# Performance work log

Hardware: AMD Instinct MI355X
Metric: run time of the kernel (lower is better)

Reference implementation:

```python
import jax, jax.numpy as jnp
import numpy as np

B, C, IC, H, W = 16, 256, 128, 32, 32  # batch, in_channels, inter_channels, spatial
EPS = 1e-5


def _conv1x1(x, w, b=None):
    # x: [B,C,H,W], w: [O,C] -> [B,O,H,W]
    y = jnp.einsum('bchw,oc->bohw', x, w)
    if b is not None:
        y = y + b[None, :, None, None]
    return y


def _dot_kernel(x, wt, wp):
    # relu-matmul attention, symmetrized, degree-rsqrt normalized with zero masking
    b, _, h, w = x.shape
    n = h * w
    t = jnp.maximum(_conv1x1(x, wt), 0.0).reshape(b, -1, n)  # [B,IC,N]
    p = jnp.maximum(_conv1x1(x, wp), 0.0).reshape(b, -1, n)  # [B,IC,N]
    att = jnp.einsum('bcn,bcm->bnm', t, p)                    # [B,N,N]
    att = (att + att.transpose(0, 2, 1)) * 0.5
    d = att.sum(axis=2)                                       # [B,N]
    dinv = jnp.where(d != 0, jax.lax.rsqrt(jnp.where(d != 0, d, 1.0)), 0.0)
    return att * dinv[:, None, :] * dinv[:, :, None]


def _bn(x, gamma, beta):
    # BatchNorm2d in training mode (batch statistics, biased variance)
    mu = jnp.mean(x, axis=(0, 2, 3), keepdims=True)
    var = jnp.mean((x - mu) ** 2, axis=(0, 2, 3), keepdims=True)
    xhat = (x - mu) * jax.lax.rsqrt(var + EPS)
    return xhat * gamma[None, :, None, None] + beta[None, :, None, None]


def setup_inputs() -> dict:
    key = jax.random.key(0)
    ks = jax.random.split(key, 32)
    s = 0.05
    inp = {
        'x':  jax.random.normal(ks[0], (B, C, H, W), jnp.float32),
        'ob': jax.random.normal(ks[1], (B, C, H, W), jnp.float32),
        'od': jax.random.normal(ks[2], (B, C, H, W), jnp.float32),
        'Wt': jax.random.normal(ks[3], (IC, C), jnp.float32) * s,
        'Wp': jax.random.normal(ks[4], (IC, C), jnp.float32) * s,
        'Wgx': jax.random.normal(ks[5], (IC, C), jnp.float32) * s,
        'bgx': jax.random.normal(ks[6], (IC,), jnp.float32) * s,
        'Wgb': jax.random.normal(ks[7], (IC, C), jnp.float32) * s,
        'bgb': jax.random.normal(ks[8], (IC,), jnp.float32) * s,
        'Wgd': jax.random.normal(ks[9], (IC, C), jnp.float32) * s,
        'bgd': jax.random.normal(ks[10], (IC,), jnp.float32) * s,
        'Wwx': jax.random.normal(ks[11], (C, IC), jnp.float32) * s,
        'bwx': jax.random.normal(ks[12], (C,), jnp.float32) * s,
        'Wwb': jax.random.normal(ks[13], (C, IC), jnp.float32) * s,
        'bwb': jax.random.normal(ks[14], (C,), jnp.float32) * s,
        'Wwd': jax.random.normal(ks[15], (C, IC), jnp.float32) * s,
        'bwd': jax.random.normal(ks[16], (C,), jnp.float32) * s,
        'Wwxb': jax.random.normal(ks[17], (C, IC), jnp.float32) * s,
        'bwxb': jax.random.normal(ks[18], (C,), jnp.float32) * s,
        'Wwxd': jax.random.normal(ks[19], (C, IC), jnp.float32) * s,
        'bwxd': jax.random.normal(ks[20], (C,), jnp.float32) * s,
        'gamma1': jnp.ones((C,), jnp.float32),
        'beta1': jnp.zeros((C,), jnp.float32),
        'gamma2': jnp.ones((C,), jnp.float32),
        'beta2': jnp.zeros((C,), jnp.float32),
        'Wout': jax.random.normal(ks[21], (C, C), jnp.float32) * s,
        'bout': jax.random.normal(ks[22], (C,), jnp.float32) * s,
    }
    return inp


def reference(x, ob, od, Wt, Wp, Wgx, bgx, Wgb, bgb, Wgd, bgd,
              Wwx, bwx, Wwb, bwb, Wwd, bwd, Wwxb, bwxb, Wwxd, bwxd,
              gamma1, beta1, gamma2, beta2, Wout, bout):
    b, c, h, w = x.shape
    n = h * w

    def g_tokens(inp, wg, bg):
        return _conv1x1(inp, wg, bg).reshape(b, -1, n).transpose(0, 2, 1)  # [B,N,IC]

    g_x = g_tokens(x, Wgx, bgx)
    g_b = g_tokens(ob, Wgb, bgb)
    g_d = g_tokens(od, Wgd, bgd)

    f_x = _dot_kernel(x, Wt, Wp)
    f_b = _dot_kernel(ob, Wt, Wp)
    f_d = _dot_kernel(od, Wt, Wp)

    def agg(f, g):
        # bmm(f,g).transpose(1,2).view(B,IC,H,W)
        return jnp.einsum('bnm,bmi->bin', f, g).reshape(b, -1, h, w)

    x_self = _conv1x1(agg(f_x, g_x), Wwx, bwx)
    ob_self = _conv1x1(agg(f_b, g_b), Wwb, bwb)
    od_self = _conv1x1(agg(f_d, g_d), Wwd, bwd)
    x_ob_cross = _conv1x1(agg(f_b, g_x), Wwxb, bwxb)
    x_od_cross = _conv1x1(agg(f_d, g_x), Wwxd, bwxd)

    od_final = _bn(od_self + x_ob_cross, gamma1, beta1)
    ob_final = _bn(ob_self + x_od_cross, gamma2, beta2)
    output = _conv1x1(od_final + ob_final + x_self, Wout, bout)
    return output + x
```

## Files before the change

### kernel.cpp

```cpp
#include <hip/hip_runtime.h>

#define GAS __attribute__((address_space(1)))
#define LAS __attribute__((address_space(3)))

typedef __attribute__((ext_vector_type(8))) short short8;
typedef __attribute__((ext_vector_type(4))) float f32x4;
typedef unsigned short u16;

constexpr int cB = 16, cC = 256, cIC = 128, cN = 1024;

__device__ __forceinline__ u16 f2bf(float v) {
    unsigned u = __builtin_bit_cast(unsigned, v);
    return (u16)((u + 0x7fffu + ((u >> 16) & 1u)) >> 16);
}
__device__ __forceinline__ float bf2f(u16 v) {
    unsigned u = ((unsigned)v) << 16;
    return __builtin_bit_cast(float, u);
}
__device__ __forceinline__ float rsz(float d) {
    return (d != 0.0f) ? rsqrtf(d) : 0.0f;
}

template<int N> __device__ __forceinline__ void wait_vmcnt() {
    if constexpr (N == 0) asm volatile("s_waitcnt vmcnt(0)" ::: "memory");
    else if constexpr (N == 1) asm volatile("s_waitcnt vmcnt(1)" ::: "memory");
    else if constexpr (N == 2) asm volatile("s_waitcnt vmcnt(2)" ::: "memory");
    else if constexpr (N == 3) asm volatile("s_waitcnt vmcnt(3)" ::: "memory");
    else if constexpr (N == 4) asm volatile("s_waitcnt vmcnt(4)" ::: "memory");
    else if constexpr (N == 5) asm volatile("s_waitcnt vmcnt(5)" ::: "memory");
    else if constexpr (N == 6) asm volatile("s_waitcnt vmcnt(6)" ::: "memory");
}

template<int BM, int BN, int WR, int WC>
__device__ __forceinline__ void gemm_core(
    const u16* __restrict__ Ab, const u16* __restrict__ Ab2, int ksplit, int lda,
    const u16* __restrict__ Bb, int ldb, int K,
    u16* lsA, u16* lsB,
    f32x4 (&acc)[BM/(WR*16)][BN/(WC*16)])
{
    constexpr int THREADS = WR * WC * 64;
    constexpr int MR = BM / (WR * 16), NR = BN / (WC * 16);
    constexpr int ACH = (BM * 64) / (THREADS * 16);
    constexpr int BCH = (BN * 64) / (THREADS * 16);
    constexpr int RPC = THREADS / 4;
    constexpr int ISSUES = ACH + BCH;

    const int tid  = threadIdx.x;
    const int lane = tid & 63;
    const int wave = tid >> 6;
    const int wr = wave / WC, wc = wave % WC;
    const int r0 = tid >> 2, slot = tid & 3;

    auto stage = [&](int buf, int kk) {
        const u16* Ak = (Ab2 != nullptr && kk >= ksplit) ? (Ab2 + (kk - ksplit)) : (Ab + kk);
        const u16* Bk = Bb + kk;
        #pragma unroll
        for (int c = 0; c < ACH; c++) {
            int row = c * RPC + r0;
            int sk = (slot ^ ((row >> 1) & 3)) << 3;
            __builtin_amdgcn_global_load_lds((GAS void*)(Ak + (size_t)row * lda + sk),
                (LAS void*)(lsA + buf * (BM * 32) + c * (THREADS * 8) + (wave << 9)), 16, 0, 0);
        }
        #pragma unroll
        for (int c = 0; c < BCH; c++) {
            int row = c * RPC + r0;
            int sk = (slot ^ ((row >> 1) & 3)) << 3;
            __builtin_amdgcn_global_load_lds((GAS void*)(Bk + (size_t)row * ldb + sk),
                (LAS void*)(lsB + buf * (BN * 32) + c * (THREADS * 8) + (wave << 9)), 16, 0, 0);
        }
    };

    stage(0, 0);
    const int nt = K >> 5;
    for (int t = 0; t < nt; t++) {
        const int cur = t & 1;
        if (t + 1 < nt) { stage(cur ^ 1, (t + 1) << 5); wait_vmcnt<ISSUES>(); }
        else            wait_vmcnt<0>();
        __builtin_amdgcn_s_barrier();
        asm volatile("" ::: "memory");

        const u16* la = lsA + cur * (BM * 32);
        const u16* lb = lsB + cur * (BN * 32);
        short8 af[MR], bf[NR];
        #pragma unroll
        for (int m = 0; m < MR; m++) {
            int row = wr * (BM / WR) + (m << 4) + (lane & 15);
            af[m] = *(const short8*)&la[(row << 5) + (((lane >> 4) ^ ((row >> 1) & 3)) << 3)];
        }
        #pragma unroll
        for (int n = 0; n < NR; n++) {
            int row = wc * (BN / WC) + (n << 4) + (lane & 15);
            bf[n] = *(const short8*)&lb[(row << 5) + (((lane >> 4) ^ ((row >> 1) & 3)) << 3)];
        }
        #pragma unroll
        for (int m = 0; m < MR; m++)
            #pragma unroll
            for (int n = 0; n < NR; n++)
                acc[m][n] = __builtin_amdgcn_mfma_f32_16x16x32_bf16(af[m], bf[n], acc[m][n], 0, 0, 0);

        asm volatile("s_waitcnt lgkmcnt(0)" ::: "memory");
        __builtin_amdgcn_sched_barrier(0);
        __builtin_amdgcn_s_barrier();
    }
}

template<int BM, int BN, int WR, int WC, bool RELU, bool OBF16, bool RBIAS, bool RESID, bool RSUM>
__global__ __launch_bounds__(WR*WC*64) void gemm_bt(
    const u16* __restrict__ A, long long sA, long long sA2, int lda,
    const u16* __restrict__ B, long long sB, long long sB2, int ldb,
    void* __restrict__ C, long long sC, long long sC2, int ldc,
    int K,
    const float* __restrict__ bias, int sb2,
    const float* __restrict__ resid, long long sR,
    float* __restrict__ rsum, int rsStride)
{
    __shared__ alignas(16) u16 lsA[2 * BM * 32];
    __shared__ alignas(16) u16 lsB[2 * BN * 32];

    const int lane = threadIdx.x & 63;
    const int wave = threadIdx.x >> 6;
    const int wr = wave / WC, wc = wave % WC;
    const int zlo = blockIdx.z & 15, zhi = blockIdx.z >> 4;

    const u16* Ab = A + zlo * sA + zhi * sA2 + (size_t)(blockIdx.x * BM) * lda;
    const u16* Bb = B + zlo * sB + zhi * sB2 + (size_t)(blockIdx.y * BN) * ldb;

    f32x4 acc[BM/(WR*16)][BN/(WC*16)] = {};
    gemm_core<BM, BN, WR, WC>(Ab, nullptr, K, lda, Bb, ldb, K, lsA, lsB, acc);

    const int rowb = blockIdx.x * BM + wr * (BM / WR) + ((lane >> 4) << 2);
    const int colb = blockIdx.y * BN + wc * (BN / WC) + (lane & 15);
    const long long cbase = zlo * sC + zhi * sC2;
    float rp[BM/(WR*16)][4] = {};
    #pragma unroll
    for (int m = 0; m < BM/(WR*16); m++) {
        #pragma unroll
        for (int n = 0; n < BN/(WC*16); n++) {
            #pragma unroll
            for (int r = 0; r < 4; r++) {
                int row = rowb + m * 16 + r;
                int col = colb + n * 16;
                float v = acc[m][n][r];
                if (RBIAS) v += bias[zhi * sb2 + row];
                if (RESID) v += resid[zlo * sR + (size_t)row * ldc + col];
                if (RELU)  v = fmaxf(v, 0.0f);
                if (RSUM)  rp[m][r] += v;
                if (OBF16) ((u16*)C)[cbase + (size_t)row * ldc + col] = f2bf(v);
                else       ((float*)C)[cbase + (size_t)row * ldc + col] = v;
            }
        }
    }
    if (RSUM) {
        #pragma unroll
        for (int m = 0; m < BM/(WR*16); m++) {
            #pragma unroll
            for (int r = 0; r < 4; r++) {
                float v = rp[m][r];
                v += __shfl_xor(v, 1, 64);
                v += __shfl_xor(v, 2, 64);
                v += __shfl_xor(v, 4, 64);
                v += __shfl_xor(v, 8, 64);
                if ((lane & 15) == 0)
                    atomicAdd(&rsum[(size_t)blockIdx.z * rsStride + rowb + m * 16 + r], v);
            }
        }
    }
}

__global__ __launch_bounds__(512) void phase2a(
    const u16* __restrict__ XT, const u16* __restrict__ WTP,
    const float* __restrict__ CS,
    u16* __restrict__ TPS, float* __restrict__ DINV)
{
    __shared__ alignas(16) u16 lsA[2 * 128 * 32];
    __shared__ alignas(16) u16 lsB[2 * 256 * 32];
    __shared__ float part[128][4];

    const int xb = blockIdx.x, zs = blockIdx.z;
    const u16* Ab = XT + (size_t)zs * 262144 + (size_t)(xb * 128) * 256;

    f32x4 acc[4][4] = {};
    gemm_core<128, 256, 2, 4>(Ab, nullptr, 256, 256, WTP, 256, 256, lsA, lsB, acc);

    const int lane = threadIdx.x & 63;
    const int wave = threadIdx.x >> 6;
    const int wr = wave >> 2, wc = wave & 3;
    const int lrow0 = wr * 64 + ((lane >> 4) << 2);
    const int colb = wc * 64 + (lane & 15);

    float wsv[4];
    #pragma unroll
    for (int n = 0; n < 4; n++) wsv[n] = 0.5f * CS[zs * 256 + ((colb + n * 16) ^ 128)];

    float pd[4][4];
    #pragma unroll
    for (int m = 0; m < 4; m++) {
        #pragma unroll
        for (int r = 0; r < 4; r++) {
            float s = 0;
            #pragma unroll
            for (int n = 0; n < 4; n++) {
                float v = fmaxf(acc[m][n][r], 0.0f);
                acc[m][n][r] = v;
                s += v * wsv[n];
            }
            pd[m][r] = s;
        }
    }
    #pragma unroll
    for (int m = 0; m < 4; m++) {
        #pragma unroll
        for (int r = 0; r < 4; r++) {
            float v = pd[m][r];
            v += __shfl_xor(v, 1, 64);
            v += __shfl_xor(v, 2, 64);
            v += __shfl_xor(v, 4, 64);
            v += __shfl_xor(v, 8, 64);
            pd[m][r] = v;
        }
    }
    if ((lane & 15) == 0) {
        #pragma unroll
        for (int m = 0; m < 4; m++)
            #pragma unroll
            for (int r = 0; r < 4; r++)
                part[lrow0 + m * 16 + r][wc] = pd[m][r];
    }
    __syncthreads();

    u16* Cb = TPS + (size_t)zs * 262144;
    float* dout = DINV + (zs << 10) + xb * 128;
    #pragma unroll
    for (int m = 0; m < 4; m++) {
        #pragma unroll
        for (int r = 0; r < 4; r++) {
            int lrow = lrow0 + m * 16 + r;
            float d = part[lrow][0] + part[lrow][1] + part[lrow][2] + part[lrow][3];
            if (wc == 0 && (lane & 15) == 0) dout[lrow] = d;
            float dv = rsz(d);
            size_t rbase = (size_t)(xb * 128 + lrow) * 256;
            #pragma unroll
            for (int n = 0; n < 4; n++)
                Cb[rbase + colb + n * 16] = f2bf(acc[m][n][r] * dv);
        }
    }
}

__global__ __launch_bounds__(512) void phase2b(
    const u16* __restrict__ XT, const u16* __restrict__ WG,
    const float* __restrict__ BG, const float* __restrict__ DINV,
    u16* __restrict__ GXp, u16* __restrict__ GBp, u16* __restrict__ GDp)
{
    __shared__ alignas(16) u16 lsA[2 * 128 * 32];
    __shared__ alignas(16) u16 lsB[2 * 256 * 32];

    const int yb = blockIdx.x, zs = blockIdx.z;
    const int stream = zs >> 4, b = zs & 15;

    const u16* Ab = WG + stream * 32768;
    const u16* Bb = XT + (size_t)zs * 262144 + (size_t)(yb * 256) * 256;

    f32x4 acc[4][4] = {};
    gemm_core<128, 256, 2, 4>(Ab, nullptr, 256, 256, Bb, 256, 256, lsA, lsB, acc);

    const int lane = threadIdx.x & 63;
    const int wave = threadIdx.x >> 6;
    const int wr = wave >> 2, wc = wave & 3;
    const int rowb = wr * 64 + ((lane >> 4) << 2);
    const int colb = yb * 256 + wc * 64 + (lane & 15);
    const float* dvx = DINV + (b << 10);
    const float* dvb = DINV + 16384 + (b << 10);
    const float* dvd = DINV + 32768 + (b << 10);
    float sx[4], sb_[4], sd[4];
    #pragma unroll
    for (int n = 0; n < 4; n++) {
        int col = colb + n * 16;
        if (stream == 0) { sx[n] = rsz(dvx[col]); sb_[n] = rsz(dvb[col]); sd[n] = rsz(dvd[col]); }
        else if (stream == 1) sb_[n] = rsz(dvb[col]);
        else sd[n] = rsz(dvd[col]);
    }
    #pragma unroll
    for (int m = 0; m < 4; m++) {
        #pragma unroll
        for (int r = 0; r < 4; r++) {
            int row = rowb + m * 16 + r;
            float bias = BG[stream * 128 + row];
            #pragma unroll
            for (int n = 0; n < 4; n++) {
                int col = colb + n * 16;
                float v = acc[m][n][r] + bias;
                if (stream == 0) {
                    GXp[(size_t)b * 131072 + ((size_t)row << 10) + col] = f2bf(v * sx[n]);
                    GBp[(size_t)b * 262144 + ((size_t)(row + 128) << 10) + col] = f2bf(v * sb_[n]);
                    GDp[(size_t)b * 262144 + ((size_t)(row + 128) << 10) + col] = f2bf(v * sd[n]);
                } else if (stream == 1) {
                    GBp[(size_t)b * 262144 + ((size_t)row << 10) + col] = f2bf(v * sb_[n]);
                } else {
                    GDp[(size_t)b * 262144 + ((size_t)row << 10) + col] = f2bf(v * sd[n]);
                }
            }
        }
    }
}

__global__ __launch_bounds__(256) void inner_gemm(
    const u16* __restrict__ TPt, const u16* __restrict__ GXp,
    const u16* __restrict__ GBp, const u16* __restrict__ GDp,
    u16* __restrict__ MX, u16* __restrict__ MB, u16* __restrict__ MD)
{
    __shared__ alignas(16) u16 lsA[2 * 128 * 32];
    __shared__ alignas(16) u16 lsB[2 * 128 * 32];

    const int z = blockIdx.z, which = z >> 4, b = z & 15;
    if (which == 0 && blockIdx.y != 0) return;
    const u16* Gp = (which == 0) ? GXp : (which == 1) ? GBp : GDp;
    u16* M = (which == 0) ? MX : (which == 1) ? MB : MD;
    const int ldc = (which == 0) ? 128 : 256;
    const long long sB = (which == 0) ? 131072 : 262144;

    const u16* Ab = TPt + (size_t)z * 262144 + (size_t)(blockIdx.x * 128) * 1024;
    const u16* Bb = Gp + (size_t)b * sB + (size_t)(blockIdx.y * 128) * 1024;

    f32x4 acc[4][4] = {};
    gemm_core<128, 128, 2, 2>(Ab, nullptr, 1024, 1024, Bb, 1024, 1024, lsA, lsB, acc);

    const int lane = threadIdx.x & 63;
    const int wave = threadIdx.x >> 6;
    const int wr = wave >> 1, wc = wave & 1;
    const int rowb = blockIdx.x * 128 + (wr << 6) + ((lane >> 4) << 2);
    const int colb = blockIdx.y * 128 + (wc << 6) + (lane & 15);
    u16* Cb = M + (size_t)b * (256 * ldc);
    #pragma unroll
    for (int m = 0; m < 4; m++)
        #pragma unroll
        for (int n = 0; n < 4; n++)
            #pragma unroll
            for (int r = 0; r < 4; r++) {
                int row = (rowb + m * 16 + r) ^ 128;
                int col = colb + n * 16;
                Cb[(size_t)row * ldc + col] = f2bf(acc[m][n][r]);
            }
}

__global__ __launch_bounds__(512) void fold_gemm(
    const u16* __restrict__ WF, const u16* __restrict__ MX,
    const u16* __restrict__ MB, const u16* __restrict__ MD,
    u16* __restrict__ FF2)
{
    __shared__ alignas(16) u16 lsA[2 * 128 * 32];
    __shared__ alignas(16) u16 lsB[2 * 256 * 32];

    const int z = blockIdx.z, q = z >> 4, b = z & 15;
    const int pr = (q == 4) ? 2 : (q >> 1);
    const int side = (q == 1 || q == 3) ? 1 : 0;
    const u16* Mp = (q == 4) ? MX : (q == 1 || q == 2) ? MB : MD;
    const int coff = (q == 1 || q == 3) ? 128 : 0;
    const int ldb  = (q == 4) ? 128 : 256;

    const u16* Ab = WF + q * 32768 + (size_t)(blockIdx.x * 128) * 128;
    const u16* Bb = Mp + (size_t)b * (256 * ldb) + coff;

    f32x4 acc[4][4] = {};
    gemm_core<128, 256, 2, 4>(Ab, nullptr, 128, 128, Bb, ldb, 128, lsA, lsB, acc);

    const int lane = threadIdx.x & 63;
    const int wave = threadIdx.x >> 6;
    const int wr = wave >> 2, wc = wave & 3;
    const int rowb = blockIdx.x * 128 + wr * 64 + ((lane >> 4) << 2);
    const int colb = side * 256 + wc * 64 + (lane & 15);
    u16* Cb = FF2 + (size_t)pr * 2097152 + (size_t)b * 131072;
    #pragma unroll
    for (int m = 0; m < 4; m++)
        #pragma unroll
        for (int n = 0; n < 4; n++)
            #pragma unroll
            for (int r = 0; r < 4; r++)
                Cb[(size_t)(rowb + m * 16 + r) * 512 + colb + n * 16] = f2bf(acc[m][n][r]);
}

__global__ __launch_bounds__(512) void outer_gemm(
    const u16* __restrict__ TPS, const u16* __restrict__ FF2,
    u16* __restrict__ SALL, float* __restrict__ BNA)
{
    __shared__ alignas(16) u16 lsA[2 * 128 * 32];
    __shared__ alignas(16) u16 lsB[2 * 256 * 32];

    const int z = blockIdx.z, zhi = z >> 4, b = z & 15;
    const int sa1[3] = {2, 1, 0}, sa2[3] = {1, 2, 0};
    const int K = (zhi == 2) ? 256 : 512;

    const u16* A1 = TPS + (size_t)(sa1[zhi] * 16 + b) * 262144 + (size_t)(blockIdx.x * 128) * 256;
    const u16* A2 = (zhi == 2) ? nullptr
                  : TPS + (size_t)(sa2[zhi] * 16 + b) * 262144 + (size_t)(blockIdx.x * 128) * 256;
    const u16* Bb = FF2 + (size_t)zhi * 2097152 + (size_t)b * 131072;

    f32x4 acc[4][4] = {};
    gemm_core<128, 256, 2, 4>(A1, A2, 256, 256, Bb, 512, K, lsA, lsB, acc);

    const int lane = threadIdx.x & 63;
    const int wave = threadIdx.x >> 6;
    const int wr = wave >> 2, wc = wave & 3;
    const int rowb = blockIdx.x * 128 + wr * 64 + ((lane >> 4) << 2);
    const int colb = wc * 64 + (lane & 15);
    u16* Cb = SALL + (size_t)b * 786432;

    float csum[4] = {}, csq[4] = {};
    #pragma unroll
    for (int m = 0; m < 4; m++)
        #pragma unroll
        for (int n = 0; n < 4; n++)
            #pragma unroll
            for (int r = 0; r < 4; r++) {
                float v = acc[m][n][r];
                Cb[(size_t)(rowb + m * 16 + r) * 768 + zhi * 256 + colb + n * 16] = f2bf(v);
                csum[n] += v;
                csq[n] += v * v;
            }
    if (zhi < 2) {
        #pragma unroll
        for (int n = 0; n < 4; n++) {
            float s = csum[n], q = csq[n];
            s += __shfl_xor(s, 16, 64); s += __shfl_xor(s, 32, 64);
            q += __shfl_xor(q, 16, 64); q += __shfl_xor(q, 32, 64);
            if (lane < 16) {
                atomicAdd(&BNA[zhi * 512 + colb + n * 16], s);
                atomicAdd(&BNA[zhi * 512 + 256 + colb + n * 16], q);
            }
        }
    }
}

__global__ __launch_bounds__(256) void bnscale(
    const float* __restrict__ Wout, const float* __restrict__ g1, const float* __restrict__ be1,
    const float* __restrict__ g2, const float* __restrict__ be2,
    const float* __restrict__ bwx, const float* __restrict__ bout,
    const float* __restrict__ BNA, u16* __restrict__ WoutS, float* __restrict__ BIAS2)
{
    int o = blockIdx.x, c = threadIdx.x;
    const float inv = 1.0f / 16384.0f;
    float m1 = BNA[c] * inv;
    float v1 = BNA[256 + c] * inv - m1 * m1;
    float sc1 = g1[c] * rsqrtf(v1 + 1e-5f), sh1 = be1[c] - m1 * sc1;
    float m2 = BNA[512 + c] * inv;
    float v2 = BNA[768 + c] * inv - m2 * m2;
    float sc2 = g2[c] * rsqrtf(v2 + 1e-5f), sh2 = be2[c] - m2 * sc2;
    float wv = Wout[o * 256 + c];
    WoutS[o * 768 + c]       = f2bf(wv * sc1);
    WoutS[o * 768 + 256 + c] = f2bf(wv * sc2);
    WoutS[o * 768 + 512 + c] = f2bf(wv);
    __shared__ float red[256];
    red[c] = wv * (sh1 + sh2 + bwx[c]);
    __syncthreads();
    for (int s = 128; s; s >>= 1) { if (c < s) red[c] += red[c + s]; __syncthreads(); }
    if (c == 0) BIAS2[o] = red[0] + bout[o];
}

__global__ void prep_transpose(const float* __restrict__ x, const float* __restrict__ ob,
                               const float* __restrict__ od, u16* __restrict__ xt,
                               const float* Wt, const float* Wp,
                               const float* Wgx, const float* Wgb, const float* Wgd,
                               const float* bgx, const float* bgb, const float* bgd,
                               const float* Wwd, const float* Wwxb, const float* Wwb,
                               const float* Wwxd, const float* Wwx,
                               u16* wtp, u16* wg, u16* wf, float* bg,
                               float* __restrict__ ZZ)
{
    int tx = threadIdx.x, ty = threadIdx.y;
    if (blockIdx.z == 48) {
        int t = (blockIdx.y * 32 + blockIdx.x) * 256 + ty * 32 + tx;
        wtp[t] = f2bf(t < 32768 ? Wt[t] : Wp[t - 32768]);
        if (t < 32768) {
            wg[t] = f2bf(Wgx[t]); wg[32768 + t] = f2bf(Wgb[t]); wg[65536 + t] = f2bf(Wgd[t]);
            wf[t]          = f2bf(0.5f * Wwd[t]);
            wf[32768 + t]  = f2bf(0.5f * Wwxb[t]);
            wf[65536 + t]  = f2bf(0.5f * Wwb[t]);
            wf[98304 + t]  = f2bf(0.5f * Wwxd[t]);
            wf[131072 + t] = f2bf(0.5f * Wwx[t]);
        }
        if (t < 384) bg[t] = (t < 128) ? bgx[t] : (t < 256) ? bgb[t - 128] : bgd[t - 256];
        if (t < 13312) ZZ[t] = 0.0f;
        return;
    }
    __shared__ float tbuf[32][33];
    int z = blockIdx.z, which = z >> 4, b = z & 15;
    const float* src = (which == 0) ? x : (which == 1) ? ob : od;
    const float* s = src + (size_t)b * cC * cN;
    u16* dst = xt + (size_t)which * (cB * cN * cC) + (size_t)b * (cN * cC);
    int n0 = blockIdx.x << 5, c0 = blockIdx.y << 5;
    #pragma unroll
    for (int i = 0; i < 4; i++) { int r = ty + (i << 3); tbuf[r][tx] = s[(size_t)(c0 + r) * cN + n0 + tx]; }
    __syncthreads();
    #pragma unroll
    for (int i = 0; i < 4; i++) { int r = ty + (i << 3); dst[(size_t)(n0 + r) * cC + c0 + tx] = f2bf(tbuf[tx][r]); }
}

extern "C" void kernel_launch(void* const* d_in, const int* in_sizes, int n_in,
                              void* d_out, int out_size, void* d_ws, size_t ws_size,
                              hipStream_t stream)
{
    const float* x    = (const float*)d_in[0];
    const float* ob   = (const float*)d_in[1];
    const float* od   = (const float*)d_in[2];
    const float* Wt   = (const float*)d_in[3];
    const float* Wp   = (const float*)d_in[4];
    const float* Wgx  = (const float*)d_in[5];
    const float* bgx  = (const float*)d_in[6];
    const float* Wgb  = (const float*)d_in[7];
    const float* bgb  = (const float*)d_in[8];
    const float* Wgd  = (const float*)d_in[9];
    const float* bgd  = (const float*)d_in[10];
    const float* Wwx  = (const float*)d_in[11];
    const float* bwx  = (const float*)d_in[12];
    const float* Wwb  = (const float*)d_in[13];
    const float* Wwd  = (const float*)d_in[15];
    const float* Wwxb = (const float*)d_in[17];
    const float* Wwxd = (const float*)d_in[19];
    const float* g1   = (const float*)d_in[21];
    const float* be1  = (const float*)d_in[22];
    const float* g2   = (const float*)d_in[23];
    const float* be2  = (const float*)d_in[24];
    const float* Wout = (const float*)d_in[25];
    const float* bout = (const float*)d_in[26];
    float* out = (float*)d_out;

    char* w = (char*)d_ws;
    u16*   XT    = (u16*)(w);
    u16*   TPt   = (u16*)(w + 25165824);
    u16*   TPS   = (u16*)(w + 50331648);
    u16*   GXp   = (u16*)(w + 75497472);
    u16*   GBp   = (u16*)(w + 79691776);
    u16*   GDp   = (u16*)(w + 88080384);
    u16*   MX    = (u16*)(w + 96468992);
    u16*   MB    = (u16*)(w + 97517568);
    u16*   MD    = (u16*)(w + 99614720);
    u16*   FF2   = (u16*)(w + 101711872);
    u16*   WTP   = (u16*)(w + 114294784);
    u16*   WG    = (u16*)(w + 114425856);
    u16*   WF    = (u16*)(w + 114622464);
    u16*   WoutS = (u16*)(w + 114950144);
    float* BGf   = (float*)(w + 115343360);
    float* BIAS2 = (float*)(w + 115345408);
    float* DINV  = (float*)(w + 115349504);
    float* ZZ    = (float*)(w + 115546112);

    float* CS  = ZZ;
    float* BNA = ZZ + 12288;
    u16*   SALL = TPt;

    prep_transpose<<<dim3(32, 8, 49), dim3(32, 8), 0, stream>>>(
        x, ob, od, XT, Wt, Wp, Wgx, Wgb, Wgd, bgx, bgb, bgd,
        Wwd, Wwxb, Wwb, Wwxd, Wwx, WTP, WG, WF, BGf, ZZ);

    gemm_bt<128, 256, 2, 4, true, true, false, false, true><<<dim3(2, 4, 48), 512, 0, stream>>>(
        WTP, 0, 0, 256,  XT, 262144, 4194304, 256,  TPt, 262144, 4194304, 1024,
        256, nullptr, 0, nullptr, 0, CS, 256);

    phase2a<<<dim3(8, 1, 48), 512, 0, stream>>>(XT, WTP, CS, TPS, DINV);

    phase2b<<<dim3(4, 1, 48), 512, 0, stream>>>(XT, WG, BGf, DINV, GXp, GBp, GDp);

    inner_gemm<<<dim3(2, 2, 48), 256, 0, stream>>>(TPt, GXp, GBp, GDp, MX, MB, MD);

    fold_gemm<<<dim3(2, 1, 80), 512, 0, stream>>>(WF, MX, MB, MD, FF2);

    outer_gemm<<<dim3(8, 1, 48), 512, 0, stream>>>(TPS, FF2, SALL, BNA);

    bnscale<<<dim3(256), 256, 0, stream>>>(Wout, g1, be1, g2, be2, bwx, bout,
                                           BNA, WoutS, BIAS2);

    gemm_bt<128, 256, 2, 4, false, false, true, true, false><<<dim3(2, 4, 16), 512, 0, stream>>>(
        WoutS, 0, 0, 768,  SALL, 786432, 0, 768,  out, 262144, 0, 1024,
        768, BIAS2, 0, x, 262144, nullptr, 0);
}
```

Before: 168.2 us.

## Restructure pipeline: merge TP GEMMs, split-K inner GEMM, move dinv scaling into outer GEMM

The two projection GEMMs (channel-major TPt and token-major TP) now run in one launch, with the degree computation moved to a separate matrix-vector kernel. The per-row rsqrt degree scaling is applied in the outer GEMM epilogue instead of being baked into TPS. The inner GEMM is split along K into two halves written side by side, and the fold GEMM absorbs that split by doubling K through a remapped B-operand addressing. The G projection and final GEMM use smaller 128x128 tiles to launch more blocks. The aim is more parallelism and fewer dependent phases, at the cost of extra kernels, more workspace traffic, and a second GEMM pass in the outer stage.

```diff
diff --git a/kernel.cpp b/kernel.cpp
--- a/kernel.cpp
+++ b/kernel.cpp
@@ -31,7 +31,7 @@
     else if constexpr (N == 6) asm volatile("s_waitcnt vmcnt(6)" ::: "memory");
 }
 
-template<int BM, int BN, int WR, int WC>
+template<int BM, int BN, int WR, int WC, bool BREMAP = false>
 __device__ __forceinline__ void gemm_core(
     const u16* __restrict__ Ab, const u16* __restrict__ Ab2, int ksplit, int lda,
     const u16* __restrict__ Bb, int ldb, int K,
@@ -53,7 +53,7 @@
 
     auto stage = [&](int buf, int kk) {
         const u16* Ak = (Ab2 != nullptr && kk >= ksplit) ? (Ab2 + (kk - ksplit)) : (Ab + kk);
-        const u16* Bk = Bb + kk;
+        const u16* Bk = Bb + (BREMAP ? (((kk >> 7) << 8) + (kk & 127)) : kk);
         #pragma unroll
         for (int c = 0; c < ACH; c++) {
             int row = c * RPC + r0;
@@ -104,15 +104,14 @@
     }
 }
 
-template<int BM, int BN, int WR, int WC, bool RELU, bool OBF16, bool RBIAS, bool RESID, bool RSUM>
+template<int BM, int BN, int WR, int WC, bool RELU, bool OBF16, bool RBIAS, bool RESID>
 __global__ __launch_bounds__(WR*WC*64) void gemm_bt(
     const u16* __restrict__ A, long long sA, long long sA2, int lda,
     const u16* __restrict__ B, long long sB, long long sB2, int ldb,
     void* __restrict__ C, long long sC, long long sC2, int ldc,
     int K,
     const float* __restrict__ bias, int sb2,
-    const float* __restrict__ resid, long long sR,
-    float* __restrict__ rsum, int rsStride)
+    const float* __restrict__ resid, long long sR)
 {
     __shared__ alignas(16) u16 lsA[2 * BM * 32];
     __shared__ alignas(16) u16 lsB[2 * BN * 32];
@@ -131,7 +130,6 @@
     const int rowb = blockIdx.x * BM + wr * (BM / WR) + ((lane >> 4) << 2);
     const int colb = blockIdx.y * BN + wc * (BN / WC) + (lane & 15);
     const long long cbase = zlo * sC + zhi * sC2;
-    float rp[BM/(WR*16)][4] = {};
     #pragma unroll
     for (int m = 0; m < BM/(WR*16); m++) {
         #pragma unroll
@@ -144,15 +142,48 @@
                 if (RBIAS) v += bias[zhi * sb2 + row];
                 if (RESID) v += resid[zlo * sR + (size_t)row * ldc + col];
                 if (RELU)  v = fmaxf(v, 0.0f);
-                if (RSUM)  rp[m][r] += v;
                 if (OBF16) ((u16*)C)[cbase + (size_t)row * ldc + col] = f2bf(v);
                 else       ((float*)C)[cbase + (size_t)row * ldc + col] = v;
             }
         }
     }
-    if (RSUM) {
-        #pragma unroll
-        for (int m = 0; m < BM/(WR*16); m++) {
+}
+
+__global__ __launch_bounds__(512) void tp_gemm(
+    const u16* __restrict__ XT, const u16* __restrict__ WTP,
+    u16* __restrict__ TPt, u16* __restrict__ TP, float* __restrict__ CS)
+{
+    __shared__ alignas(16) u16 lsA[2 * 128 * 32];
+    __shared__ alignas(16) u16 lsB[2 * 256 * 32];
+
+    const int id = blockIdx.x;
+    const int lane = threadIdx.x & 63;
+    const int wave = threadIdx.x >> 6;
+    const int wr = wave >> 2, wc = wave & 3;
+
+    if (id < 384) {
+        const int z = id >> 3, r_ = id & 7, cx = r_ >> 2, ny = r_ & 3;
+        const u16* Ab = WTP + (size_t)(cx * 128) * 256;
+        const u16* Bb = XT + (size_t)z * 262144 + (size_t)(ny * 256) * 256;
+        f32x4 acc[4][4] = {};
+        gemm_core<128, 256, 2, 4>(Ab, nullptr, 256, 256, Bb, 256, 256, lsA, lsB, acc);
+
+        const int rowb = cx * 128 + wr * 64 + ((lane >> 4) << 2);
+        const int colb = ny * 256 + wc * 64 + (lane & 15);
+        u16* Cb = TPt + (size_t)z * 262144;
+        float rp[4][4] = {};
+        #pragma unroll
+        for (int m = 0; m < 4; m++)
+            #pragma unroll
+            for (int n = 0; n < 4; n++)
+                #pragma unroll
+                for (int r = 0; r < 4; r++) {
+                    float v = fmaxf(acc[m][n][r], 0.0f);
+                    Cb[(size_t)(rowb + m * 16 + r) * 1024 + colb + n * 16] = f2bf(v);
+                    rp[m][r] += v;
+                }
+        #pragma unroll
+        for (int m = 0; m < 4; m++)
             #pragma unroll
             for (int r = 0; r < 4; r++) {
                 float v = rp[m][r];
@@ -161,113 +192,66 @@
                 v += __shfl_xor(v, 4, 64);
                 v += __shfl_xor(v, 8, 64);
                 if ((lane & 15) == 0)
-                    atomicAdd(&rsum[(size_t)blockIdx.z * rsStride + rowb + m * 16 + r], v);
+                    atomicAdd(&CS[z * 256 + rowb + m * 16 + r], v);
             }
-        }
-    }
-}
-
-__global__ __launch_bounds__(512) void phase2a(
-    const u16* __restrict__ XT, const u16* __restrict__ WTP,
-    const float* __restrict__ CS,
-    u16* __restrict__ TPS, float* __restrict__ DINV)
-{
-    __shared__ alignas(16) u16 lsA[2 * 128 * 32];
-    __shared__ alignas(16) u16 lsB[2 * 256 * 32];
-    __shared__ float part[128][4];
-
-    const int xb = blockIdx.x, zs = blockIdx.z;
-    const u16* Ab = XT + (size_t)zs * 262144 + (size_t)(xb * 128) * 256;
-
-    f32x4 acc[4][4] = {};
-    gemm_core<128, 256, 2, 4>(Ab, nullptr, 256, 256, WTP, 256, 256, lsA, lsB, acc);
-
-    const int lane = threadIdx.x & 63;
-    const int wave = threadIdx.x >> 6;
-    const int wr = wave >> 2, wc = wave & 3;
-    const int lrow0 = wr * 64 + ((lane >> 4) << 2);
-    const int colb = wc * 64 + (lane & 15);
-
-    float wsv[4];
-    #pragma unroll
-    for (int n = 0; n < 4; n++) wsv[n] = 0.5f * CS[zs * 256 + ((colb + n * 16) ^ 128)];
-
-    float pd[4][4];
-    #pragma unroll
-    for (int m = 0; m < 4; m++) {
-        #pragma unroll
-        for (int r = 0; r < 4; r++) {
-            float s = 0;
-            #pragma unroll
-            for (int n = 0; n < 4; n++) {
-                float v = fmaxf(acc[m][n][r], 0.0f);
-                acc[m][n][r] = v;
-                s += v * wsv[n];
-            }
-            pd[m][r] = s;
-        }
-    }
-    #pragma unroll
-    for (int m = 0; m < 4; m++) {
-        #pragma unroll
-        for (int r = 0; r < 4; r++) {
-            float v = pd[m][r];
-            v += __shfl_xor(v, 1, 64);
-            v += __shfl_xor(v, 2, 64);
-            v += __shfl_xor(v, 4, 64);
-            v += __shfl_xor(v, 8, 64);
-            pd[m][r] = v;
-        }
-    }
-    if ((lane & 15) == 0) {
+    } else {
+        const int id2 = id - 384;
+        const int z = id2 >> 3, nx = id2 & 7;
+        const u16* Ab = XT + (size_t)z * 262144 + (size_t)(nx * 128) * 256;
+        f32x4 acc[4][4] = {};
+        gemm_core<128, 256, 2, 4>(Ab, nullptr, 256, 256, WTP, 256, 256, lsA, lsB, acc);
+
+        const int rowb = nx * 128 + wr * 64 + ((lane >> 4) << 2);
+        const int colb = wc * 64 + (lane & 15);
+        u16* Cb = TP + (size_t)z * 262144;
         #pragma unroll
         for (int m = 0; m < 4; m++)
             #pragma unroll
-            for (int r = 0; r < 4; r++)
-                part[lrow0 + m * 16 + r][wc] = pd[m][r];
-    }
+            for (int n = 0; n < 4; n++)
+                #pragma unroll
+                for (int r = 0; r < 4; r++)
+                    Cb[(size_t)(rowb + m * 16 + r) * 256 + colb + n * 16] =
+                        f2bf(fmaxf(acc[m][n][r], 0.0f));
+    }
+}
+
+__global__ __launch_bounds__(256) void dinv_mv(
+    const u16* __restrict__ TPt, const float* __restrict__ CS, float* __restrict__ DINV)
+{
+    const int z = blockIdx.y;
+    const int n = blockIdx.x * 256 + threadIdx.x;
+    __shared__ float ws[256];
+    ws[threadIdx.x] = 0.5f * CS[z * 256 + (threadIdx.x ^ 128)];
     __syncthreads();
-
-    u16* Cb = TPS + (size_t)zs * 262144;
-    float* dout = DINV + (zs << 10) + xb * 128;
-    #pragma unroll
-    for (int m = 0; m < 4; m++) {
-        #pragma unroll
-        for (int r = 0; r < 4; r++) {
-            int lrow = lrow0 + m * 16 + r;
-            float d = part[lrow][0] + part[lrow][1] + part[lrow][2] + part[lrow][3];
-            if (wc == 0 && (lane & 15) == 0) dout[lrow] = d;
-            float dv = rsz(d);
-            size_t rbase = (size_t)(xb * 128 + lrow) * 256;
-            #pragma unroll
-            for (int n = 0; n < 4; n++)
-                Cb[rbase + colb + n * 16] = f2bf(acc[m][n][r] * dv);
-        }
-    }
-}
-
-__global__ __launch_bounds__(512) void phase2b(
+    const u16* base = TPt + (size_t)z * 262144 + n;
+    float d = 0;
+    #pragma unroll 8
+    for (int c = 0; c < 256; c++) d += bf2f(base[(size_t)c << 10]) * ws[c];
+    DINV[(z << 10) + n] = d;
+}
+
+__global__ __launch_bounds__(256) void g_gemm(
     const u16* __restrict__ XT, const u16* __restrict__ WG,
     const float* __restrict__ BG, const float* __restrict__ DINV,
     u16* __restrict__ GXp, u16* __restrict__ GBp, u16* __restrict__ GDp)
 {
     __shared__ alignas(16) u16 lsA[2 * 128 * 32];
-    __shared__ alignas(16) u16 lsB[2 * 256 * 32];
+    __shared__ alignas(16) u16 lsB[2 * 128 * 32];
 
     const int yb = blockIdx.x, zs = blockIdx.z;
     const int stream = zs >> 4, b = zs & 15;
 
     const u16* Ab = WG + stream * 32768;
-    const u16* Bb = XT + (size_t)zs * 262144 + (size_t)(yb * 256) * 256;
+    const u16* Bb = XT + (size_t)zs * 262144 + (size_t)(yb * 128) * 256;
 
     f32x4 acc[4][4] = {};
-    gemm_core<128, 256, 2, 4>(Ab, nullptr, 256, 256, Bb, 256, 256, lsA, lsB, acc);
+    gemm_core<128, 128, 2, 2>(Ab, nullptr, 256, 256, Bb, 256, 256, lsA, lsB, acc);
 
     const int lane = threadIdx.x & 63;
     const int wave = threadIdx.x >> 6;
-    const int wr = wave >> 2, wc = wave & 3;
-    const int rowb = wr * 64 + ((lane >> 4) << 2);
-    const int colb = yb * 256 + wc * 64 + (lane & 15);
+    const int wr = wave >> 1, wc = wave & 1;
+    const int rowb = (wr << 6) + ((lane >> 4) << 2);
+    const int colb = yb * 128 + (wc << 6) + (lane & 15);
     const float* dvx = DINV + (b << 10);
     const float* dvb = DINV + 16384 + (b << 10);
     const float* dvd = DINV + 32768 + (b << 10);
@@ -303,7 +287,7 @@
     }
 }
 
-__global__ __launch_bounds__(256) void inner_gemm(
+__global__ __launch_bounds__(256) void inner_splitk(
     const u16* __restrict__ TPt, const u16* __restrict__ GXp,
     const u16* __restrict__ GBp, const u16* __restrict__ GDp,
     u16* __restrict__ MX, u16* __restrict__ MB, u16* __restrict__ MD)
@@ -311,18 +295,21 @@
     __shared__ alignas(16) u16 lsA[2 * 128 * 32];
     __shared__ alignas(16) u16 lsB[2 * 128 * 32];
 
-    const int z = blockIdx.z, which = z >> 4, b = z & 15;
-    if (which == 0 && blockIdx.y != 0) return;
+    const int bz = blockIdx.z;
+    const int split = bz / 48, z = bz % 48;
+    const int which = z >> 4, b = z & 15;
+    if (which == 0 && blockIdx.y) return;
     const u16* Gp = (which == 0) ? GXp : (which == 1) ? GBp : GDp;
     u16* M = (which == 0) ? MX : (which == 1) ? MB : MD;
-    const int ldc = (which == 0) ? 128 : 256;
+    const int JD  = (which == 0) ? 128 : 256;
+    const int ldc = 2 * JD;
     const long long sB = (which == 0) ? 131072 : 262144;
 
-    const u16* Ab = TPt + (size_t)z * 262144 + (size_t)(blockIdx.x * 128) * 1024;
-    const u16* Bb = Gp + (size_t)b * sB + (size_t)(blockIdx.y * 128) * 1024;
+    const u16* Ab = TPt + (size_t)z * 262144 + (size_t)(blockIdx.x * 128) * 1024 + split * 512;
+    const u16* Bb = Gp + (size_t)b * sB + (size_t)(blockIdx.y * 128) * 1024 + split * 512;
 
     f32x4 acc[4][4] = {};
-    gemm_core<128, 128, 2, 2>(Ab, nullptr, 1024, 1024, Bb, 1024, 1024, lsA, lsB, acc);
+    gemm_core<128, 128, 2, 2>(Ab, nullptr, 512, 1024, Bb, 1024, 512, lsA, lsB, acc);
 
     const int lane = threadIdx.x & 63;
     const int wave = threadIdx.x >> 6;
@@ -337,13 +324,13 @@
             #pragma unroll
             for (int r = 0; r < 4; r++) {
                 int row = (rowb + m * 16 + r) ^ 128;
-                int col = colb + n * 16;
+                int col = split * JD + colb + n * 16;
                 Cb[(size_t)row * ldc + col] = f2bf(acc[m][n][r]);
             }
 }
 
 __global__ __launch_bounds__(512) void fold_gemm(
-    const u16* __restrict__ WF, const u16* __restrict__ MX,
+    const u16* __restrict__ WF2, const u16* __restrict__ MX,
     const u16* __restrict__ MB, const u16* __restrict__ MD,
     u16* __restrict__ FF2)
 {
@@ -353,57 +340,90 @@
     const int z = blockIdx.z, q = z >> 4, b = z & 15;
     const int pr = (q == 4) ? 2 : (q >> 1);
     const int side = (q == 1 || q == 3) ? 1 : 0;
-    const u16* Mp = (q == 4) ? MX : (q == 1 || q == 2) ? MB : MD;
-    const int coff = (q == 1 || q == 3) ? 128 : 0;
-    const int ldb  = (q == 4) ? 128 : 256;
-
-    const u16* Ab = WF + q * 32768 + (size_t)(blockIdx.x * 128) * 128;
-    const u16* Bb = Mp + (size_t)b * (256 * ldb) + coff;
+
+    const u16* Ab = WF2 + q * 65536 + (size_t)(blockIdx.x * 128) * 256;
 
     f32x4 acc[4][4] = {};
-    gemm_core<128, 256, 2, 4>(Ab, nullptr, 128, 128, Bb, ldb, 128, lsA, lsB, acc);
-
-    const int lane = threadIdx.x & 63;
-    const int wave = threadIdx.x >> 6;
-    const int wr = wave >> 2, wc = wave & 3;
-    const int rowb = blockIdx.x * 128 + wr * 64 + ((lane >> 4) << 2);
-    const int colb = side * 256 + wc * 64 + (lane & 15);
-    u16* Cb = FF2 + (size_t)pr * 2097152 + (size_t)b * 131072;
-    #pragma unroll
-    for (int m = 0; m < 4; m++)
-        #pragma unroll
-        for (int n = 0; n < 4; n++)
-            #pragma unroll
-            for (int r = 0; r < 4; r++)
-                Cb[(size_t)(rowb + m * 16 + r) * 512 + colb + n * 16] = f2bf(acc[m][n][r]);
-}
-
-__global__ __launch_bounds__(512) void outer_gemm(
-    const u16* __restrict__ TPS, const u16* __restrict__ FF2,
-    u16* __restrict__ SALL, float* __restrict__ BNA)
-{
-    __shared__ alignas(16) u16 lsA[2 * 128 * 32];
-    __shared__ alignas(16) u16 lsB[2 * 256 * 32];
-
-    const int z = blockIdx.z, zhi = z >> 4, b = z & 15;
-    const int sa1[3] = {2, 1, 0}, sa2[3] = {1, 2, 0};
-    const int K = (zhi == 2) ? 256 : 512;
-
-    const u16* A1 = TPS + (size_t)(sa1[zhi] * 16 + b) * 262144 + (size_t)(blockIdx.x * 128) * 256;
-    const u16* A2 = (zhi == 2) ? nullptr
-                  : TPS + (size_t)(sa2[zhi] * 16 + b) * 262144 + (size_t)(blockIdx.x * 128) * 256;
-    const u16* Bb = FF2 + (size_t)zhi * 2097152 + (size_t)b * 131072;
-
-    f32x4 acc[4][4] = {};
-    gemm_core<128, 256, 2, 4>(A1, A2, 256, 256, Bb, 512, K, lsA, lsB, acc);
+    if (q == 4) {
+        const u16* Bb = MX + (size_t)b * 65536;
+        gemm_core<128, 256, 2, 4, false>(Ab, nullptr, 256, 256, Bb, 256, 256, lsA, lsB, acc);
+    } else {
+        const u16* Mp = (q == 1 || q == 2) ? MB : MD;
+        const int coff = side ? 128 : 0;
+        const u16* Bb = Mp + (size_t)b * 131072 + coff;
+        gemm_core<128, 256, 2, 4, true>(Ab, nullptr, 256, 256, Bb, 512, 256, lsA, lsB, acc);
+    }
 
     const int lane = threadIdx.x & 63;
     const int wave = threadIdx.x >> 6;
     const int wr = wave >> 2, wc = wave & 3;
     const int rowb = blockIdx.x * 128 + wr * 64 + ((lane >> 4) << 2);
     const int colb = wc * 64 + (lane & 15);
+    u16* Cb = FF2 + (size_t)pr * 2097152 + (size_t)b * 131072;
+    #pragma unroll
+    for (int m = 0; m < 4; m++)
+        #pragma unroll
+        for (int n = 0; n < 4; n++)
+            #pragma unroll
+            for (int r = 0; r < 4; r++)
+                Cb[(size_t)(rowb + m * 16 + r) * 512 + side * 256 + colb + n * 16]
+                    = f2bf(acc[m][n][r]);
+}
+
+__global__ __launch_bounds__(512) void outer_gemm(
+    const u16* __restrict__ TP, const u16* __restrict__ FF2,
+    const float* __restrict__ DINV,
+    u16* __restrict__ SALL, float* __restrict__ BNA)
+{
+    __shared__ alignas(16) u16 lsA[2 * 128 * 32];
+    __shared__ alignas(16) u16 lsB[2 * 256 * 32];
+
+    const int z = blockIdx.z, zhi = z >> 4, b = z & 15;
+    const int sa1[3] = {2, 1, 0}, sa2[3] = {1, 2, 0};
+
+    const int lane = threadIdx.x & 63;
+    const int wave = threadIdx.x >> 6;
+    const int wr = wave >> 2, wc = wave & 3;
+    const int rowb = blockIdx.x * 128 + wr * 64 + ((lane >> 4) << 2);
+    const int colb = wc * 64 + (lane & 15);
+
+    const u16* A1 = TP + (size_t)(sa1[zhi] * 16 + b) * 262144 + (size_t)(blockIdx.x * 128) * 256;
+    const u16* B1 = FF2 + (size_t)zhi * 2097152 + (size_t)b * 131072;
+    const float* dv1 = DINV + sa1[zhi] * 16384 + (b << 10);
+
+    f32x4 acc[4][4] = {};
+    gemm_core<128, 256, 2, 4>(A1, nullptr, 256, 256, B1, 512, 256, lsA, lsB, acc);
+
+    f32x4 keep[4][4];
+    #pragma unroll
+    for (int m = 0; m < 4; m++) {
+        f32x4 dva;
+        #pragma unroll
+        for (int r = 0; r < 4; r++) dva[r] = rsz(dv1[rowb + m * 16 + r]);
+        #pragma unroll
+        for (int n = 0; n < 4; n++) keep[m][n] = acc[m][n] * dva;
+    }
+
+    if (zhi < 2) {
+        const u16* A2 = TP + (size_t)(sa2[zhi] * 16 + b) * 262144 + (size_t)(blockIdx.x * 128) * 256;
+        const u16* B2 = B1 + 256;
+        const float* dv2 = DINV + sa2[zhi] * 16384 + (b << 10);
+        #pragma unroll
+        for (int m = 0; m < 4; m++)
+            #pragma unroll
+            for (int n = 0; n < 4; n++) acc[m][n] = f32x4{0.f, 0.f, 0.f, 0.f};
+        gemm_core<128, 256, 2, 4>(A2, nullptr, 256, 256, B2, 512, 256, lsA, lsB, acc);
+        #pragma unroll
+        for (int m = 0; m < 4; m++) {
+            f32x4 dva;
+            #pragma unroll
+            for (int r = 0; r < 4; r++) dva[r] = rsz(dv2[rowb + m * 16 + r]);
+            #pragma unroll
+            for (int n = 0; n < 4; n++) keep[m][n] = keep[m][n] + acc[m][n] * dva;
+        }
+    }
+
     u16* Cb = SALL + (size_t)b * 786432;
-
     float csum[4] = {}, csq[4] = {};
     #pragma unroll
     for (int m = 0; m < 4; m++)
@@ -411,7 +431,7 @@
         for (int n = 0; n < 4; n++)
             #pragma unroll
             for (int r = 0; r < 4; r++) {
-                float v = acc[m][n][r];
+                float v = keep[m][n][r];
                 Cb[(size_t)(rowb + m * 16 + r) * 768 + zhi * 256 + colb + n * 16] = f2bf(v);
                 csum[n] += v;
                 csq[n] += v * v;
@@ -462,7 +482,7 @@
                                const float* bgx, const float* bgb, const float* bgd,
                                const float* Wwd, const float* Wwxb, const float* Wwb,
                                const float* Wwxd, const float* Wwx,
-                               u16* wtp, u16* wg, u16* wf, float* bg,
+                               u16* wtp, u16* wg, u16* wf2, float* bg,
                                float* __restrict__ ZZ)
 {
     int tx = threadIdx.x, ty = threadIdx.y;
@@ -471,11 +491,13 @@
         wtp[t] = f2bf(t < 32768 ? Wt[t] : Wp[t - 32768]);
         if (t < 32768) {
             wg[t] = f2bf(Wgx[t]); wg[32768 + t] = f2bf(Wgb[t]); wg[65536 + t] = f2bf(Wgd[t]);
-            wf[t]          = f2bf(0.5f * Wwd[t]);
-            wf[32768 + t]  = f2bf(0.5f * Wwxb[t]);
-            wf[65536 + t]  = f2bf(0.5f * Wwb[t]);
-            wf[98304 + t]  = f2bf(0.5f * Wwxd[t]);
-            wf[131072 + t] = f2bf(0.5f * Wwx[t]);
+        }
+        {
+            int o = t >> 8, k = t & 255, j = k & 127;
+            const float* Wq[5] = {Wwd, Wwxb, Wwb, Wwxd, Wwx};
+            #pragma unroll
+            for (int q = 0; q < 5; q++)
+                wf2[q * 65536 + t] = f2bf(0.5f * Wq[q][o * 128 + j]);
         }
         if (t < 384) bg[t] = (t < 128) ? bgx[t] : (t < 256) ? bgb[t - 128] : bgd[t - 256];
         if (t < 13312) ZZ[t] = 0.0f;
@@ -526,49 +548,47 @@
     char* w = (char*)d_ws;
     u16*   XT    = (u16*)(w);
     u16*   TPt   = (u16*)(w + 25165824);
-    u16*   TPS   = (u16*)(w + 50331648);
+    u16*   TP    = (u16*)(w + 50331648);
     u16*   GXp   = (u16*)(w + 75497472);
     u16*   GBp   = (u16*)(w + 79691776);
     u16*   GDp   = (u16*)(w + 88080384);
     u16*   MX    = (u16*)(w + 96468992);
-    u16*   MB    = (u16*)(w + 97517568);
-    u16*   MD    = (u16*)(w + 99614720);
-    u16*   FF2   = (u16*)(w + 101711872);
-    u16*   WTP   = (u16*)(w + 114294784);
-    u16*   WG    = (u16*)(w + 114425856);
-    u16*   WF    = (u16*)(w + 114622464);
-    u16*   WoutS = (u16*)(w + 114950144);
-    float* BGf   = (float*)(w + 115343360);
-    float* BIAS2 = (float*)(w + 115345408);
-    float* DINV  = (float*)(w + 115349504);
-    float* ZZ    = (float*)(w + 115546112);
-
-    float* CS  = ZZ;
-    float* BNA = ZZ + 12288;
+    u16*   MB    = (u16*)(w + 98566144);
+    u16*   MD    = (u16*)(w + 102760448);
+    u16*   FF2   = (u16*)(w + 106954752);
+    u16*   WTP   = (u16*)(w + 119537664);
+    u16*   WG    = (u16*)(w + 119668736);
+    u16*   WF2   = (u16*)(w + 119865344);
+    u16*   WoutS = (u16*)(w + 120520704);
+    float* BGf   = (float*)(w + 120913920);
+    float* BIAS2 = (float*)(w + 120915968);
+    float* DINV  = (float*)(w + 120920064);
+    float* ZZ    = (float*)(w + 121116672);
+
+    float* CS   = ZZ;
+    float* BNA  = ZZ + 12288;
     u16*   SALL = TPt;
 
     prep_transpose<<<dim3(32, 8, 49), dim3(32, 8), 0, stream>>>(
         x, ob, od, XT, Wt, Wp, Wgx, Wgb, Wgd, bgx, bgb, bgd,
-        Wwd, Wwxb, Wwb, Wwxd, Wwx, WTP, WG, WF, BGf, ZZ);
-
-    gemm_bt<128, 256, 2, 4, true, true, false, false, true><<<dim3(2, 4, 48), 512, 0, stream>>>(
-        WTP, 0, 0, 256,  XT, 262144, 4194304, 256,  TPt, 262144, 4194304, 1024,
-        256, nullptr, 0, nullptr, 0, CS, 256);
-
-    phase2a<<<dim3(8, 1, 48), 512, 0, stream>>>(XT, WTP, CS, TPS, DINV);
-
-    phase2b<<<dim3(4, 1, 48), 512, 0, stream>>>(XT, WG, BGf, DINV, GXp, GBp, GDp);
-
-    inner_gemm<<<dim3(2, 2, 48), 256, 0, stream>>>(TPt, GXp, GBp, GDp, MX, MB, MD);
-
-    fold_gemm<<<dim3(2, 1, 80), 512, 0, stream>>>(WF, MX, MB, MD, FF2);
-
-    outer_gemm<<<dim3(8, 1, 48), 512, 0, stream>>>(TPS, FF2, SALL, BNA);
+        Wwd, Wwxb, Wwb, Wwxd, Wwx, WTP, WG, WF2, BGf, ZZ);
+
+    tp_gemm<<<dim3(768), 512, 0, stream>>>(XT, WTP, TPt, TP, CS);
+
+    dinv_mv<<<dim3(4, 48), 256, 0, stream>>>(TPt, CS, DINV);
+
+    g_gemm<<<dim3(8, 1, 48), 256, 0, stream>>>(XT, WG, BGf, DINV, GXp, GBp, GDp);
+
+    inner_splitk<<<dim3(2, 2, 96), 256, 0, stream>>>(TPt, GXp, GBp, GDp, MX, MB, MD);
+
+    fold_gemm<<<dim3(2, 1, 80), 512, 0, stream>>>(WF2, MX, MB, MD, FF2);
+
+    outer_gemm<<<dim3(8, 1, 48), 512, 0, stream>>>(TP, FF2, DINV, SALL, BNA);
 
     bnscale<<<dim3(256), 256, 0, stream>>>(Wout, g1, be1, g2, be2, bwx, bout,
                                            BNA, WoutS, BIAS2);
 
-    gemm_bt<128, 256, 2, 4, false, false, true, true, false><<<dim3(2, 4, 16), 512, 0, stream>>>(
+    gemm_bt<128, 128, 2, 2, false, false, true, true><<<dim3(2, 8, 16), 256, 0, stream>>>(
         WoutS, 0, 0, 768,  SALL, 786432, 0, 768,  out, 262144, 0, 1024,
-        768, BIAS2, 0, x, 262144, nullptr, 0);
-}
+        768, BIAS2, 0, x, 262144);
+}
```

After: 167.3 us. About the same (-0.6%).
